# Performance work log

Measured on AMD Instinct MI355X. Metric: run time of the kernel, lower is better.

## Reference

```python
import jax, jax.numpy as jnp
import numpy as np

DIM = 4096
N_HEADS = 32
HEAD_DIM = 128
N_KV = 8
REP = N_HEADS // N_KV  # 4
B = 8       # number of packed sequences (block-diagonal blocks)
S = 1024    # tokens per sequence
T = B * S   # seqlen_sum = 8192


def setup_inputs() -> dict:
    key = jax.random.key(0)
    ks = jax.random.split(key, 6)
    x = jax.random.normal(ks[0], (T, DIM), dtype=jnp.float32)
    # RoPE freqs: positions restart at 0 for each packed sequence
    pos = jnp.tile(jnp.arange(S, dtype=jnp.float32), B)            # [T]
    inv_freq = 1.0 / (10000.0 ** (jnp.arange(0, HEAD_DIM, 2, dtype=jnp.float32) / HEAD_DIM))  # [HEAD_DIM//2]
    freqs = pos[:, None] * inv_freq[None, :]                       # [T, HEAD_DIM//2]
    cos = jnp.cos(freqs)
    sin = jnp.sin(freqs)
    s = 0.02
    wq = jax.random.normal(ks[1], (DIM, N_HEADS * HEAD_DIM), dtype=jnp.float32) * s
    wk = jax.random.normal(ks[2], (DIM, N_KV * HEAD_DIM), dtype=jnp.float32) * s
    wv = jax.random.normal(ks[3], (DIM, N_KV * HEAD_DIM), dtype=jnp.float32) * s
    wo = jax.random.normal(ks[4], (N_HEADS * HEAD_DIM, DIM), dtype=jnp.float32) * s
    return {"x": x, "cos": cos, "sin": sin, "wq": wq, "wk": wk, "wv": wv, "wo": wo}


def _rope(t, cos, sin):
    # t: [T, H, D]; cos/sin: [T, D//2]; complex rotation on (even, odd) pairs
    th, hd = t.shape[1], t.shape[2]
    tp = t.reshape(t.shape[0], th, hd // 2, 2)
    te, to = tp[..., 0], tp[..., 1]
    c = cos[:, None, :]
    s = sin[:, None, :]
    oe = te * c - to * s
    oo = te * s + to * c
    return jnp.stack([oe, oo], axis=-1).reshape(t.shape)


def reference(x, cos, sin, wq, wk, wv, wo):
    scale = HEAD_DIM ** -0.5
    q = (x @ wq).reshape(T, N_HEADS, HEAD_DIM)
    k = (x @ wk).reshape(T, N_KV, HEAD_DIM)
    v = (x @ wv).reshape(T, N_KV, HEAD_DIM)
    q = _rope(q, cos, sin)
    k = _rope(k, cos, sin)
    # Block-diagonal mask with equal blocks == batched attention over B sequences.
    # GQA: q head index h = kv*REP + r (matches repeat_interleave on kv dim),
    # so group q heads as [N_KV, REP] instead of materializing repeated K/V.
    q = q.reshape(B, S, N_KV, REP, HEAD_DIM)
    k = k.reshape(B, S, N_KV, HEAD_DIM)
    v = v.reshape(B, S, N_KV, HEAD_DIM)
    scores = jnp.einsum('bqkrd,bskd->bkrqs', q, k) * scale   # [B, N_KV, REP, S, S]
    attn = jax.nn.softmax(scores, axis=-1)
    out = jnp.einsum('bkrqs,bskd->bqkrd', attn, v)           # [B, S, N_KV, REP, D]
    out = out.reshape(T, N_HEADS * HEAD_DIM)
    return out @ wo
```

## Files before the change

kernel.cpp:

```cpp
#include <hip/hip_runtime.h>
#include <math.h>

typedef unsigned short ushort_t;
typedef __attribute__((ext_vector_type(8))) short short8;
typedef __attribute__((ext_vector_type(4))) float f32x4;

#define MFMA16(a, b, c) __builtin_amdgcn_mfma_f32_16x16x32_bf16(a, b, c, 0, 0, 0)

__device__ __forceinline__ ushort_t f2bf(float f) {
    union { float f; unsigned u; } v;
    v.f = f;
    unsigned r = v.u + 0x7FFF + ((v.u >> 16) & 1);
    return (ushort_t)(r >> 16);
}

__device__ __forceinline__ void gload_lds16(const ushort_t* g, ushort_t* l) {
    __builtin_amdgcn_global_load_lds(
        (const __attribute__((address_space(1))) void*)g,
        (__attribute__((address_space(3))) void*)l, 16, 0, 0);
}

__global__ __launch_bounds__(256) void cast_f32_bf16(const float* __restrict__ src,
                                                     ushort_t* __restrict__ dst, int n8) {
    int i = blockIdx.x * 256 + threadIdx.x;
    if (i >= n8) return;
    const float4* s = (const float4*)src;
    float4 a = s[2 * i], b = s[2 * i + 1];
    union { ushort_t u[8]; uint4 v; } o;
    o.u[0] = f2bf(a.x); o.u[1] = f2bf(a.y); o.u[2] = f2bf(a.z); o.u[3] = f2bf(a.w);
    o.u[4] = f2bf(b.x); o.u[5] = f2bf(b.y); o.u[6] = f2bf(b.z); o.u[7] = f2bf(b.w);
    ((uint4*)dst)[i] = o.v;
}

__global__ __launch_bounds__(256) void transpose_cast(const float* __restrict__ src,
                                                      int D, int N,
                                                      ushort_t* __restrict__ dst, int dstStride) {
    __shared__ float t[32][33];
    int n0 = blockIdx.x * 32, d0 = blockIdx.y * 32;
    int tx = threadIdx.x & 31, ty = threadIdx.x >> 5;
#pragma unroll
    for (int i = 0; i < 4; i++)
        t[ty + 8 * i][tx] = src[(size_t)(d0 + ty + 8 * i) * N + n0 + tx];
    __syncthreads();
#pragma unroll
    for (int i = 0; i < 4; i++) {
        int n = ty + 8 * i;
        dst[(size_t)(n0 + n) * dstStride + d0 + tx] = f2bf(t[tx][n]);
    }
}

__global__ __launch_bounds__(256) void transpose_v(const ushort_t* __restrict__ qkv,
                                                   ushort_t* __restrict__ vt) {
    __shared__ ushort_t t[32][33];
    int bk = blockIdx.z; int b = bk >> 3, kvh = bk & 7;
    int s0 = blockIdx.x * 32, d0 = blockIdx.y * 32;
    int tx = threadIdx.x & 31, ty = threadIdx.x >> 5;
#pragma unroll
    for (int i = 0; i < 4; i++)
        t[ty + 8 * i][tx] = qkv[(size_t)(b * 1024 + s0 + ty + 8 * i) * 6144 + 5120 + kvh * 128 + d0 + tx];
    __syncthreads();
#pragma unroll
    for (int i = 0; i < 4; i++)
        vt[((size_t)(b * 8 + kvh) * 128 + d0 + ty + 8 * i) * 1024 + s0 + tx] = t[tx][ty + 8 * i];
}

template <int EPI>
__global__ __launch_bounds__(512, 2) void gemm8p(
    const ushort_t* __restrict__ A, const ushort_t* __restrict__ Bt,
    ushort_t* __restrict__ obf, float* __restrict__ of32,
    int M, int N, int K,
    const float* __restrict__ cosT, const float* __restrict__ sinT) {
    extern __shared__ __align__(16) ushort_t lds[];
    const int tid = threadIdx.x;
    const int lane = tid & 63, wv = tid >> 6;
    const int wr = wv >> 2, wc = wv & 3;
    const int lr = lane & 15, g = lane >> 4;

    const int gx = gridDim.x;
    const int nwg = gx * gridDim.y;
    const int bid = blockIdx.y * gx + blockIdx.x;
    const int swz = (bid & 7) * (nwg >> 3) + (bid >> 3);
    const int brow = (swz / gx) * 256, bcol = (swz % gx) * 256;

    const int row_st = tid >> 2;
    const int pslot  = tid & 3;
    const int lsrc   = ((pslot - ((row_st >> 2) & 3)) & 3) ^ (row_st & 3);
    const size_t aSrc0 = (size_t)(brow + row_st) * K + lsrc * 8;
    const size_t bSrc0 = (size_t)(bcol + row_st) * K + lsrc * 8;

    const int prd = ((g ^ (lr & 3)) + ((lr >> 2) & 3)) & 3;
    const int aRd = wr * 4096 + lr * 32 + prd * 8;
    const int bRd = 32768 + wc * 2048 + lr * 32 + prd * 8;

    f32x4 acc[8][4];
#pragma unroll
    for (int m = 0; m < 8; m++)
#pragma unroll
        for (int n = 0; n < 4; n++) acc[m][n] = (f32x4){0.f, 0.f, 0.f, 0.f};

#define STAGE_A(kn)                                                                  \
    {                                                                                \
        const int s_ = (kn) & 3;                                                     \
        gload_lds16(A + aSrc0 + (size_t)(kn) * 32, lds + s_ * 8192 + wv * 512);      \
        gload_lds16(A + aSrc0 + (size_t)128 * K + (size_t)(kn) * 32,                 \
                    lds + s_ * 8192 + 4096 + wv * 512);                              \
    }
#define STAGE_B(kn)                                                                  \
    {                                                                                \
        const int s_ = (kn) & 3;                                                     \
        gload_lds16(Bt + bSrc0 + (size_t)(kn) * 32, lds + 32768 + s_ * 8192 + wv * 512); \
        gload_lds16(Bt + bSrc0 + (size_t)128 * K + (size_t)(kn) * 32,                \
                    lds + 32768 + s_ * 8192 + 4096 + wv * 512);                      \
    }

    STAGE_A(0); STAGE_B(0);
    STAGE_A(1); STAGE_B(1);
    STAGE_A(2); STAGE_B(2);

    const int NKS = K >> 5;
    for (int ks = 0; ks < NKS; ++ks) {
        const int s = ks & 3;
        if (ks < NKS - 2)       asm volatile("s_waitcnt vmcnt(8)" ::: "memory");
        else if (ks == NKS - 2) asm volatile("s_waitcnt vmcnt(4)" ::: "memory");
        else                    asm volatile("s_waitcnt vmcnt(0)" ::: "memory");
        __builtin_amdgcn_s_barrier();
        __builtin_amdgcn_sched_barrier(0);

        short8 bfr[4], af[4];
#pragma unroll
        for (int n = 0; n < 4; ++n)
            bfr[n] = *(const short8*)(lds + s * 8192 + bRd + n * 512);
#pragma unroll
        for (int m = 0; m < 4; ++m)
            af[m] = *(const short8*)(lds + s * 8192 + aRd + m * 512);
        if (ks < NKS - 3) STAGE_A(ks + 3);
        __builtin_amdgcn_sched_barrier(0);
        __builtin_amdgcn_s_setprio(1);
#pragma unroll
        for (int m = 0; m < 4; ++m)
#pragma unroll
            for (int n = 0; n < 4; ++n)
                acc[m][n] = MFMA16(af[m], bfr[n], acc[m][n]);
        __builtin_amdgcn_s_setprio(0);

        __builtin_amdgcn_s_barrier();
        __builtin_amdgcn_sched_barrier(0);
#pragma unroll
        for (int m = 0; m < 4; ++m)
            af[m] = *(const short8*)(lds + s * 8192 + aRd + 2048 + m * 512);
        if (ks < NKS - 3) STAGE_B(ks + 3);
        __builtin_amdgcn_sched_barrier(0);
        __builtin_amdgcn_s_setprio(1);
#pragma unroll
        for (int m = 0; m < 4; ++m)
#pragma unroll
            for (int n = 0; n < 4; ++n)
                acc[m + 4][n] = MFMA16(af[m], bfr[n], acc[m + 4][n]);
        __builtin_amdgcn_s_setprio(0);
    }
#undef STAGE_A
#undef STAGE_B

#pragma unroll
    for (int m = 0; m < 8; ++m) {
#pragma unroll
        for (int n = 0; n < 4; ++n) {
#pragma unroll
            for (int reg = 0; reg < 4; ++reg) {
                int r = brow + wr * 128 + m * 16 + g * 4 + reg;
                int c = bcol + wc * 64 + n * 16 + lr;
                float val = acc[m][n][reg];
                if (EPI == 1) {
                    float other = __shfl_xor(val, 1, 64);
                    if (c < 5120) {
                        int pos = r & 1023;
                        int pair = (c & 127) >> 1;
                        float cz = cosT[pos * 64 + pair];
                        float sz = sinT[pos * 64 + pair];
                        val = val * cz + other * ((c & 1) ? sz : -sz);
                        if (c < 4096) val *= 0.12752551286084110f;
                    }
                    obf[(size_t)r * N + c] = f2bf(val);
                } else {
                    of32[(size_t)r * N + c] = val;
                }
            }
        }
    }
}

__global__ __launch_bounds__(512, 2) void attn_fwd2(const ushort_t* __restrict__ qkv,
                                                    const ushort_t* __restrict__ vt,
                                                    ushort_t* __restrict__ aout) {
    extern __shared__ __align__(16) ushort_t lds[];
    const int tid = threadIdx.x, lane = tid & 63, w = tid >> 6;
    const int lr = lane & 15, g = lane >> 4;
    const int hr = w & 3, qc = w >> 2;
    const int qt = blockIdx.x, kvh = blockIdx.y, b = blockIdx.z;
    const int h = kvh * 4 + hr;
    const size_t qRow0 = (size_t)b * 1024 + qt * 64 + qc * 32;
    const size_t kBase = (size_t)b * 1024 * 6144 + 4096 + kvh * 128;
    const size_t vBase = (size_t)(b * 8 + kvh) * 128 * 1024;
    ushort_t* Pw = lds + 32768 + w * 2304;

    short8 qf[2][4];
#pragma unroll
    for (int qg = 0; qg < 2; ++qg)
#pragma unroll
        for (int kd = 0; kd < 4; ++kd)
            qf[qg][kd] = *(const short8*)&qkv[(qRow0 + qg * 16 + lr) * 6144 + h * 128 + kd * 32 + g * 8];

    f32x4 o[2][8];
#pragma unroll
    for (int qg = 0; qg < 2; ++qg)
#pragma unroll
        for (int nd = 0; nd < 8; ++nd) o[qg][nd] = (f32x4){0.f, 0.f, 0.f, 0.f};
    f32x4 lsum[2];
    lsum[0] = (f32x4){0.f, 0.f, 0.f, 0.f};
    lsum[1] = (f32x4){0.f, 0.f, 0.f, 0.f};

#define STAGE_KV(kt)                                                                   \
    {                                                                                  \
        const int buf_ = (kt) & 1;                                                     \
        {                                                                              \
            const int r0_ = tid >> 4, p_ = tid & 15;                                   \
            gload_lds16(qkv + kBase + (size_t)((kt) * 64 + r0_) * 6144 + ((p_ ^ (r0_ & 7)) * 8), \
                        lds + buf_ * 8192 + r0_ * 128 + p_ * 8);                       \
            const int r1_ = r0_ + 32;                                                  \
            gload_lds16(qkv + kBase + (size_t)((kt) * 64 + r1_) * 6144 + ((p_ ^ (r1_ & 7)) * 8), \
                        lds + buf_ * 8192 + r1_ * 128 + p_ * 8);                       \
        }                                                                              \
        {                                                                              \
            const int d0_ = tid >> 3, p_ = tid & 7;                                    \
            gload_lds16(vt + vBase + (size_t)d0_ * 1024 + (kt) * 64 + ((p_ ^ (d0_ & 7)) * 8), \
                        lds + 16384 + buf_ * 8192 + d0_ * 64 + p_ * 8);                \
            const int d1_ = d0_ + 64;                                                  \
            gload_lds16(vt + vBase + (size_t)d1_ * 1024 + (kt) * 64 + ((p_ ^ (d1_ & 7)) * 8), \
                        lds + 16384 + buf_ * 8192 + d1_ * 64 + p_ * 8);                \
        }                                                                              \
    }

    STAGE_KV(0);

    for (int kt = 0; kt < 16; ++kt) {
        const int buf = kt & 1;
        if (kt < 15) {
            STAGE_KV(kt + 1);
            asm volatile("s_waitcnt vmcnt(4)" ::: "memory");
        } else {
            asm volatile("s_waitcnt vmcnt(0)" ::: "memory");
        }
        __builtin_amdgcn_s_barrier();

        f32x4 sc[2][4];
#pragma unroll
        for (int qg = 0; qg < 2; ++qg)
#pragma unroll
            for (int ns = 0; ns < 4; ++ns) sc[qg][ns] = (f32x4){0.f, 0.f, 0.f, 0.f};
        __builtin_amdgcn_s_setprio(1);
#pragma unroll
        for (int ns = 0; ns < 4; ++ns) {
            const int key = ns * 16 + lr;
#pragma unroll
            for (int kd = 0; kd < 4; ++kd) {
                const short8 kf = *(const short8*)(lds + buf * 8192 + key * 128 +
                                                   (((kd * 4 + g) ^ (lr & 7)) * 8));
                sc[0][ns] = MFMA16(qf[0][kd], kf, sc[0][ns]);
                sc[1][ns] = MFMA16(qf[1][kd], kf, sc[1][ns]);
            }
        }
        __builtin_amdgcn_s_setprio(0);

#pragma unroll
        for (int qg = 0; qg < 2; ++qg) {
#pragma unroll
            for (int ns = 0; ns < 4; ++ns) {
#pragma unroll
                for (int j = 0; j < 4; ++j) {
                    float p = exp2f(sc[qg][ns][j]);
                    sc[qg][ns][j] = p;
                    lsum[qg][j] += p;
                }
            }
        }
#pragma unroll
        for (int qg = 0; qg < 2; ++qg)
#pragma unroll
            for (int ns = 0; ns < 4; ++ns)
#pragma unroll
                for (int j = 0; j < 4; ++j)
                    Pw[(qg * 16 + g * 4 + j) * 72 + ns * 16 + lr] = f2bf(sc[qg][ns][j]);

        __builtin_amdgcn_s_setprio(1);
#pragma unroll
        for (int ks = 0; ks < 2; ++ks) {
            short8 pa[2];
            pa[0] = *(const short8*)(Pw + (0 + lr) * 72 + ks * 32 + g * 8);
            pa[1] = *(const short8*)(Pw + (16 + lr) * 72 + ks * 32 + g * 8);
#pragma unroll
            for (int nd = 0; nd < 8; ++nd) {
                const int d = nd * 16 + lr;
                const short8 vf = *(const short8*)(lds + 16384 + buf * 8192 + d * 64 +
                                                   (((ks * 4 + g) ^ (d & 7)) * 8));
                o[0][nd] = MFMA16(pa[0], vf, o[0][nd]);
                o[1][nd] = MFMA16(pa[1], vf, o[1][nd]);
            }
        }
        __builtin_amdgcn_s_setprio(0);
        __builtin_amdgcn_s_barrier();
    }
#undef STAGE_KV

#pragma unroll
    for (int qg = 0; qg < 2; ++qg) {
#pragma unroll
        for (int j = 0; j < 4; ++j) {
            float s = lsum[qg][j];
            s += __shfl_xor(s, 1, 64);
            s += __shfl_xor(s, 2, 64);
            s += __shfl_xor(s, 4, 64);
            s += __shfl_xor(s, 8, 64);
            const float inv = 1.0f / s;
            const size_t r = qRow0 + qg * 16 + g * 4 + j;
#pragma unroll
            for (int nd = 0; nd < 8; ++nd)
                aout[r * 4096 + h * 128 + nd * 16 + lr] = f2bf(o[qg][nd][j] * inv);
        }
    }
}

extern "C" void kernel_launch(void* const* d_in, const int* in_sizes, int n_in,
                              void* d_out, int out_size, void* d_ws, size_t ws_size,
                              hipStream_t stream) {
    const float* x    = (const float*)d_in[0];
    const float* cosT = (const float*)d_in[1];
    const float* sinT = (const float*)d_in[2];
    const float* wq   = (const float*)d_in[3];
    const float* wk   = (const float*)d_in[4];
    const float* wv   = (const float*)d_in[5];
    const float* wo   = (const float*)d_in[6];
    float* out = (float*)d_out;

    char* ws = (char*)d_ws;
    ushort_t* xb   = (ushort_t*)(ws);
    ushort_t* wT   = (ushort_t*)(ws + 67108864);
    ushort_t* woT  = (ushort_t*)(ws + 117440512);
    ushort_t* qkv  = (ushort_t*)(ws + 150994944);
    ushort_t* vtb  = (ushort_t*)(ws + 67108864);
    ushort_t* attn = (ushort_t*)(ws);

    hipFuncSetAttribute((const void*)gemm8p<1>, hipFuncAttributeMaxDynamicSharedMemorySize, 131072);
    hipFuncSetAttribute((const void*)gemm8p<2>, hipFuncAttributeMaxDynamicSharedMemorySize, 131072);
    hipFuncSetAttribute((const void*)attn_fwd2, hipFuncAttributeMaxDynamicSharedMemorySize, 102400);

    cast_f32_bf16<<<16384, 256, 0, stream>>>(x, xb, 8192 * 4096 / 8);
    transpose_cast<<<dim3(128, 128), 256, 0, stream>>>(wq, 4096, 4096, wT, 4096);
    transpose_cast<<<dim3(32, 128), 256, 0, stream>>>(wk, 4096, 1024, wT + (size_t)4096 * 4096, 4096);
    transpose_cast<<<dim3(32, 128), 256, 0, stream>>>(wv, 4096, 1024, wT + (size_t)5120 * 4096, 4096);
    transpose_cast<<<dim3(128, 128), 256, 0, stream>>>(wo, 4096, 4096, woT, 4096);

    gemm8p<1><<<dim3(24, 32), 512, 131072, stream>>>(xb, wT, qkv, nullptr, 8192, 6144, 4096, cosT, sinT);
    transpose_v<<<dim3(32, 4, 64), 256, 0, stream>>>(qkv, vtb);
    attn_fwd2<<<dim3(16, 8, 8), 512, 102400, stream>>>(qkv, vtb, attn);
    gemm8p<2><<<dim3(16, 32), 512, 131072, stream>>>(attn, woT, nullptr, out, 8192, 4096, 4096, nullptr, nullptr);
}
```

Baseline: 981.3 us.

## Restructure GEMM mainloop to double-buffered 64-wide K tiles with XOR swizzle

Changes the GEMM K-step from 32 to 64 per LDS tile, replacing the 4-stage 32-wide ring with a 2-stage double buffer of 64-wide tiles. It switches to an 8-way XOR swizzle so LDS reads avoid bank conflicts. Loads for the next tile are spread across four MFMA sub-phases per iteration, which halves the loop trip count and the barrier count per unit of K. The catch is a shallower prefetch: only one tile is in flight, which may expose more global-load latency than the old three-tile lookahead.

```diff
diff --git a/kernel.cpp b/kernel.cpp
--- a/kernel.cpp
+++ b/kernel.cpp
@@ -65,7 +65,7 @@
 }
 
 template <int EPI>
-__global__ __launch_bounds__(512, 2) void gemm8p(
+__global__ __launch_bounds__(512, 2) void gemm8x(
     const ushort_t* __restrict__ A, const ushort_t* __restrict__ Bt,
     ushort_t* __restrict__ obf, float* __restrict__ of32,
     int M, int N, int K,
@@ -82,15 +82,16 @@
     const int swz = (bid & 7) * (nwg >> 3) + (bid >> 3);
     const int brow = (swz / gx) * 256, bcol = (swz % gx) * 256;
 
-    const int row_st = tid >> 2;
-    const int pslot  = tid & 3;
-    const int lsrc   = ((pslot - ((row_st >> 2) & 3)) & 3) ^ (row_st & 3);
-    const size_t aSrc0 = (size_t)(brow + row_st) * K + lsrc * 8;
-    const size_t bSrc0 = (size_t)(bcol + row_st) * K + lsrc * 8;
-
-    const int prd = ((g ^ (lr & 3)) + ((lr >> 2) & 3)) & 3;
-    const int aRd = wr * 4096 + lr * 32 + prd * 8;
-    const int bRd = 32768 + wc * 2048 + lr * 32 + prd * 8;
+    const int st_r = tid >> 3, st_p = tid & 7;
+    const int cA = (st_p ^ (st_r & 7)) * 8;
+    const size_t aS0 = (size_t)(brow + st_r) * K + cA;
+    const size_t bS0 = (size_t)(bcol + st_r) * K + cA;
+    const int dstT = st_r * 64 + st_p * 8;
+
+    const int sl0 = (g ^ (lr & 7)) * 8;
+    const int sl1 = ((4 + g) ^ (lr & 7)) * 8;
+    const int aRow = (wr * 128 + lr) * 64;
+    const int bRow = (wc * 64 + lr) * 64;
 
     f32x4 acc[8][4];
 #pragma unroll
@@ -98,42 +99,35 @@
 #pragma unroll
         for (int n = 0; n < 4; n++) acc[m][n] = (f32x4){0.f, 0.f, 0.f, 0.f};
 
-#define STAGE_A(kn)                                                                  \
-    {                                                                                \
-        const int s_ = (kn) & 3;                                                     \
-        gload_lds16(A + aSrc0 + (size_t)(kn) * 32, lds + s_ * 8192 + wv * 512);      \
-        gload_lds16(A + aSrc0 + (size_t)128 * K + (size_t)(kn) * 32,                 \
-                    lds + s_ * 8192 + 4096 + wv * 512);                              \
-    }
-#define STAGE_B(kn)                                                                  \
-    {                                                                                \
-        const int s_ = (kn) & 3;                                                     \
-        gload_lds16(Bt + bSrc0 + (size_t)(kn) * 32, lds + 32768 + s_ * 8192 + wv * 512); \
-        gload_lds16(Bt + bSrc0 + (size_t)128 * K + (size_t)(kn) * 32,                \
-                    lds + 32768 + s_ * 8192 + 4096 + wv * 512);                      \
-    }
-
-    STAGE_A(0); STAGE_B(0);
-    STAGE_A(1); STAGE_B(1);
-    STAGE_A(2); STAGE_B(2);
-
-    const int NKS = K >> 5;
-    for (int ks = 0; ks < NKS; ++ks) {
-        const int s = ks & 3;
-        if (ks < NKS - 2)       asm volatile("s_waitcnt vmcnt(8)" ::: "memory");
-        else if (ks == NKS - 2) asm volatile("s_waitcnt vmcnt(4)" ::: "memory");
-        else                    asm volatile("s_waitcnt vmcnt(0)" ::: "memory");
-        __builtin_amdgcn_s_barrier();
-        __builtin_amdgcn_sched_barrier(0);
-
+#define STG_A(kn, roff)                                                          \
+    gload_lds16(A + aS0 + (size_t)(roff) * K + (size_t)(kn) * 64,                \
+                lds + ((kn) & 1) * 16384 + (roff) * 64 + dstT)
+#define STG_B(kn, roff)                                                          \
+    gload_lds16(Bt + bS0 + (size_t)(roff) * K + (size_t)(kn) * 64,               \
+                lds + 32768 + ((kn) & 1) * 16384 + (roff) * 64 + dstT)
+
+    STG_B(0, 0);  STG_B(0, 64);
+    STG_B(0, 128); STG_B(0, 192);
+    STG_A(0, 0);  STG_A(0, 128);
+    STG_A(0, 64); STG_A(0, 192);
+
+    const int NKT = K >> 6;
+    for (int kt = 0; kt < NKT; ++kt) {
+        const int buf = (kt & 1) * 16384;
+        const bool stg = kt < NKT - 1;
+        const int kn = kt + 1;
         short8 bfr[4], af[4];
+
+        asm volatile("s_waitcnt vmcnt(2)" ::: "memory");
+        __builtin_amdgcn_s_barrier();
+        __builtin_amdgcn_sched_barrier(0);
 #pragma unroll
         for (int n = 0; n < 4; ++n)
-            bfr[n] = *(const short8*)(lds + s * 8192 + bRd + n * 512);
-#pragma unroll
-        for (int m = 0; m < 4; ++m)
-            af[m] = *(const short8*)(lds + s * 8192 + aRd + m * 512);
-        if (ks < NKS - 3) STAGE_A(ks + 3);
+            bfr[n] = *(const short8*)(lds + 32768 + buf + bRow + n * 1024 + sl0);
+#pragma unroll
+        for (int m = 0; m < 4; ++m)
+            af[m] = *(const short8*)(lds + buf + aRow + m * 1024 + sl0);
+        if (stg) { STG_B(kn, 0); STG_B(kn, 64); }
         __builtin_amdgcn_sched_barrier(0);
         __builtin_amdgcn_s_setprio(1);
 #pragma unroll
@@ -143,12 +137,14 @@
                 acc[m][n] = MFMA16(af[m], bfr[n], acc[m][n]);
         __builtin_amdgcn_s_setprio(0);
 
-        __builtin_amdgcn_s_barrier();
-        __builtin_amdgcn_sched_barrier(0);
-#pragma unroll
-        for (int m = 0; m < 4; ++m)
-            af[m] = *(const short8*)(lds + s * 8192 + aRd + 2048 + m * 512);
-        if (ks < NKS - 3) STAGE_B(ks + 3);
+        if (kt == NKT - 1) asm volatile("s_waitcnt vmcnt(0)" ::: "memory");
+        else               asm volatile("s_waitcnt vmcnt(2)" ::: "memory");
+        __builtin_amdgcn_s_barrier();
+        __builtin_amdgcn_sched_barrier(0);
+#pragma unroll
+        for (int m = 0; m < 4; ++m)
+            af[m] = *(const short8*)(lds + buf + aRow + 4096 + m * 1024 + sl0);
+        if (stg) { STG_B(kn, 128); STG_B(kn, 192); }
         __builtin_amdgcn_sched_barrier(0);
         __builtin_amdgcn_s_setprio(1);
 #pragma unroll
@@ -157,9 +153,42 @@
             for (int n = 0; n < 4; ++n)
                 acc[m + 4][n] = MFMA16(af[m], bfr[n], acc[m + 4][n]);
         __builtin_amdgcn_s_setprio(0);
-    }
-#undef STAGE_A
-#undef STAGE_B
+
+        __builtin_amdgcn_s_barrier();
+        __builtin_amdgcn_sched_barrier(0);
+#pragma unroll
+        for (int n = 0; n < 4; ++n)
+            bfr[n] = *(const short8*)(lds + 32768 + buf + bRow + n * 1024 + sl1);
+#pragma unroll
+        for (int m = 0; m < 4; ++m)
+            af[m] = *(const short8*)(lds + buf + aRow + m * 1024 + sl1);
+        if (stg) { STG_A(kn, 0); STG_A(kn, 128); }
+        __builtin_amdgcn_sched_barrier(0);
+        __builtin_amdgcn_s_setprio(1);
+#pragma unroll
+        for (int m = 0; m < 4; ++m)
+#pragma unroll
+            for (int n = 0; n < 4; ++n)
+                acc[m][n] = MFMA16(af[m], bfr[n], acc[m][n]);
+        __builtin_amdgcn_s_setprio(0);
+
+        __builtin_amdgcn_s_barrier();
+        __builtin_amdgcn_sched_barrier(0);
+#pragma unroll
+        for (int m = 0; m < 4; ++m)
+            af[m] = *(const short8*)(lds + buf + aRow + 4096 + m * 1024 + sl1);
+        if (stg) { STG_A(kn, 64); STG_A(kn, 192); }
+        __builtin_amdgcn_sched_barrier(0);
+        __builtin_amdgcn_s_setprio(1);
+#pragma unroll
+        for (int m = 0; m < 4; ++m)
+#pragma unroll
+            for (int n = 0; n < 4; ++n)
+                acc[m + 4][n] = MFMA16(af[m], bfr[n], acc[m + 4][n]);
+        __builtin_amdgcn_s_setprio(0);
+    }
+#undef STG_A
+#undef STG_B
 
 #pragma unroll
     for (int m = 0; m < 8; ++m) {
@@ -349,8 +378,8 @@
     ushort_t* vtb  = (ushort_t*)(ws + 67108864);
     ushort_t* attn = (ushort_t*)(ws);
 
-    hipFuncSetAttribute((const void*)gemm8p<1>, hipFuncAttributeMaxDynamicSharedMemorySize, 131072);
-    hipFuncSetAttribute((const void*)gemm8p<2>, hipFuncAttributeMaxDynamicSharedMemorySize, 131072);
+    hipFuncSetAttribute((const void*)gemm8x<1>, hipFuncAttributeMaxDynamicSharedMemorySize, 131072);
+    hipFuncSetAttribute((const void*)gemm8x<2>, hipFuncAttributeMaxDynamicSharedMemorySize, 131072);
     hipFuncSetAttribute((const void*)attn_fwd2, hipFuncAttributeMaxDynamicSharedMemorySize, 102400);
 
     cast_f32_bf16<<<16384, 256, 0, stream>>>(x, xb, 8192 * 4096 / 8);
@@ -359,8 +388,8 @@
     transpose_cast<<<dim3(32, 128), 256, 0, stream>>>(wv, 4096, 1024, wT + (size_t)5120 * 4096, 4096);
     transpose_cast<<<dim3(128, 128), 256, 0, stream>>>(wo, 4096, 4096, woT, 4096);
 
-    gemm8p<1><<<dim3(24, 32), 512, 131072, stream>>>(xb, wT, qkv, nullptr, 8192, 6144, 4096, cosT, sinT);
+    gemm8x<1><<<dim3(24, 32), 512, 131072, stream>>>(xb, wT, qkv, nullptr, 8192, 6144, 4096, cosT, sinT);
     transpose_v<<<dim3(32, 4, 64), 256, 0, stream>>>(qkv, vtb);
     attn_fwd2<<<dim3(16, 8, 8), 512, 102400, stream>>>(qkv, vtb, attn);
-    gemm8p<2><<<dim3(16, 32), 512, 131072, stream>>>(attn, woT, nullptr, out, 8192, 4096, 4096, nullptr, nullptr);
-}
+    gemm8x<2><<<dim3(16, 32), 512, 131072, stream>>>(attn, woT, nullptr, out, 8192, 4096, 4096, nullptr, nullptr);
+}
```

Result: faster. 940.8 us (-4.1%).
